# Kernel optimization log

Measured on AMD Instinct MI355X. Metric: run time of the kernel, lower is better.

Reference implementation:

```python
import jax, jax.numpy as jnp
import numpy as np

B, N, M = 4, 8192, 8192


def setup_inputs() -> dict:
    key = jax.random.key(0)
    k1, k2 = jax.random.split(key)
    xyz1 = jax.random.normal(k1, (B, N, 3), dtype=jnp.float32)
    xyz2 = jax.random.normal(k2, (B, M, 3), dtype=jnp.float32)
    return {"xyz1": xyz1, "xyz2": xyz2}


def reference(xyz1, xyz2):
    # Note: torch.cdist(p=2) returns sqrt(sq); min over sqrt == min over sq
    # (monotone), and the module squares afterward, so min of squared
    # distances is exactly equivalent (and avoids sqrt-at-0 grad issues).
    sq1 = jnp.sum(xyz1 * xyz1, axis=-1)  # (B, N)
    sq2 = jnp.sum(xyz2 * xyz2, axis=-1)  # (B, M)
    cross = jnp.einsum("bnd,bmd->bnm", xyz1, xyz2)  # (B, N, M)
    d2 = jnp.maximum(sq1[:, :, None] + sq2[:, None, :] - 2.0 * cross, 0.0)
    dist1 = jnp.min(d2, axis=2)  # (B, N) nearest in xyz2 for each xyz1 point
    dist2 = jnp.min(d2, axis=1)  # (B, M) nearest in xyz1 for each xyz2 point
    return jnp.mean(dist1) + jnp.mean(dist2)
```

## Files before the change

### kernel.cpp

```cpp
#include <hip/hip_runtime.h>
#include <math.h>

typedef short  bf16x8 __attribute__((ext_vector_type(8)));
typedef float  f32x16 __attribute__((ext_vector_type(16)));

constexpr int BATCH = 4, NPTS = 8192;
constexpr int CLOUD = BATCH * NPTS;

__device__ inline unsigned short bf16_rne(float x) {
    unsigned int u = __float_as_uint(x);
    return (unsigned short)((u + 0x7FFFu + ((u >> 16) & 1u)) >> 16);
}
__device__ inline float bf16_val(unsigned short h) {
    return __uint_as_float(((unsigned int)h) << 16);
}

__global__ __launch_bounds__(256) void cd_prep(
    const float* __restrict__ x1, const float* __restrict__ x2,
    uint4* __restrict__ APK, uint4* __restrict__ BPK,
    unsigned int* __restrict__ dist) {
    const int i = blockIdx.x * 256 + threadIdx.x;
    dist[i] = 0x7F800000u;
    const float* src = (i < CLOUD) ? x1 : x2;
    const int idx = i & (CLOUD - 1);
    const float x = src[idx*3+0], y = src[idx*3+1], z = src[idx*3+2];
    const float r = x*x + y*y + z*z;

    const unsigned short one = 0x3F80u;
    const unsigned short r0 = bf16_rne(r);
    const float rm1 = r - bf16_val(r0);
    const unsigned short r1 = bf16_rne(rm1);
    const unsigned short r2 = bf16_rne(rm1 - bf16_val(r1));

    const unsigned short hx = bf16_rne(x), hy = bf16_rne(y), hz = bf16_rne(z);
    const unsigned short lx = bf16_rne(x - bf16_val(hx));
    const unsigned short ly = bf16_rne(y - bf16_val(hy));
    const unsigned short lz = bf16_rne(z - bf16_val(hz));
    uint4 a0, a1;
    a0.x = (unsigned)hx | ((unsigned)lx << 16);
    a0.y = (unsigned)hx | ((unsigned)hy << 16);
    a0.z = (unsigned)ly | ((unsigned)hy << 16);
    a0.w = (unsigned)hz | ((unsigned)lz << 16);
    a1.x = (unsigned)hz | ((unsigned)one << 16);
    a1.y = (unsigned)one | ((unsigned)one << 16);
    a1.z = (unsigned)r0 | ((unsigned)r1 << 16);
    a1.w = (unsigned)r2;
    APK[2*i+0] = a0;  APK[2*i+1] = a1;

    const float tx = -2.f*x, ty = -2.f*y, tz = -2.f*z;
    const unsigned short ax = bf16_rne(tx), ay = bf16_rne(ty), az = bf16_rne(tz);
    const unsigned short bx = bf16_rne(tx - bf16_val(ax));
    const unsigned short by = bf16_rne(ty - bf16_val(ay));
    const unsigned short bz = bf16_rne(tz - bf16_val(az));
    uint4 b0, b1;
    b0.x = (unsigned)ax | ((unsigned)ax << 16);
    b0.y = (unsigned)bx | ((unsigned)ay << 16);
    b0.z = (unsigned)ay | ((unsigned)by << 16);
    b0.w = (unsigned)az | ((unsigned)az << 16);
    b1.x = (unsigned)bz | ((unsigned)r0 << 16);
    b1.y = (unsigned)r1 | ((unsigned)r2 << 16);
    b1.z = (unsigned)one | ((unsigned)one << 16);
    b1.w = (unsigned)one;
    BPK[2*i+0] = b0;  BPK[2*i+1] = b1;
}

__global__ __launch_bounds__(256) void cd_gemm(
    const uint4* __restrict__ APK, const uint4* __restrict__ BPK,
    unsigned int* __restrict__ dist) {

    __shared__ float lbuf[4][32][33];

    const int tid = threadIdx.x;
    const int wv  = tid >> 6;
    const int l   = tid & 63;
    const int lane31 = l & 31, half = l >> 5;

    const int wid = blockIdx.x * 4 + wv;
    const int dir = wid >> 12;
    const int b   = (wid >> 10) & 3;
    const int cc  = (wid >> 7) & 7;
    const int rg  = wid & 127;

    const int aBase = (dir ? CLOUD : 0) + b * NPTS + rg * 64;
    const int bBase = (dir ? 0 : CLOUD) + b * NPTS + cc * 1024;

    bf16x8 afr0, afr1;
    {
        uint4 v0 = APK[(size_t)(aBase + lane31) * 2 + half];
        uint4 v1 = APK[(size_t)(aBase + 32 + lane31) * 2 + half];
        __builtin_memcpy(&afr0, &v0, 16);
        __builtin_memcpy(&afr1, &v1, 16);
    }

    f32x16 zc;
#pragma unroll
    for (int i = 0; i < 16; ++i) zc[i] = 0.0f;

    float racc[2][16];
#pragma unroll
    for (int f = 0; f < 2; ++f)
#pragma unroll
        for (int r = 0; r < 16; ++r) racc[f][r] = INFINITY;

    uint4 u0, v0, u1, v1;
    const size_t bofs = (size_t)(bBase + lane31) * 2 + half;
#define CD_LD(U, V, PR) \
    U = BPK[bofs + (PR) * 128]; V = BPK[bofs + (PR) * 128 + 64];
#define CD_COMP(U, V)                                                        \
    {                                                                        \
        bf16x8 ba, bb;                                                       \
        __builtin_memcpy(&ba, &U, 16);                                       \
        __builtin_memcpy(&bb, &V, 16);                                       \
        f32x16 c0 = __builtin_amdgcn_mfma_f32_32x32x16_bf16(afr0, ba, zc, 0, 0, 0); \
        f32x16 c1 = __builtin_amdgcn_mfma_f32_32x32x16_bf16(afr0, bb, zc, 0, 0, 0); \
        f32x16 c2 = __builtin_amdgcn_mfma_f32_32x32x16_bf16(afr1, ba, zc, 0, 0, 0); \
        f32x16 c3 = __builtin_amdgcn_mfma_f32_32x32x16_bf16(afr1, bb, zc, 0, 0, 0); \
        _Pragma("unroll")                                                    \
        for (int r = 0; r < 16; ++r) {                                       \
            racc[0][r] = fminf(fminf(c0[r], c1[r]), racc[0][r]);             \
            racc[1][r] = fminf(fminf(c2[r], c3[r]), racc[1][r]);             \
        }                                                                    \
    }

    CD_LD(u0, v0, 0);
    for (int p = 0; p < 14; p += 2) {
        CD_LD(u1, v1, p + 1);
        CD_COMP(u0, v0);
        CD_LD(u0, v0, p + 2);
        CD_COMP(u1, v1);
    }
    CD_LD(u1, v1, 15);
    CD_COMP(u0, v0);
    CD_COMP(u1, v1);
#undef CD_LD
#undef CD_COMP

    const int distBase = dir * CLOUD + b * NPTS + rg * 64;
#pragma unroll
    for (int f = 0; f < 2; ++f) {
#pragma unroll
        for (int r = 0; r < 16; ++r) {
            const int rl = (r & 3) + 8 * (r >> 2) + 4 * half;
            lbuf[wv][rl][lane31] = racc[f][r];
        }
        const int row = l >> 1;
        float m = INFINITY;
#pragma unroll
        for (int i = 0; i < 16; ++i)
            m = fminf(m, lbuf[wv][row][(l & 1) * 16 + i]);
        m = fminf(m, __shfl_xor(m, 1, 64));
        if ((l & 1) == 0)
            atomicMin(&dist[distBase + f * 32 + row],
                      __float_as_uint(fmaxf(m, 0.0f)));
    }
}

__global__ __launch_bounds__(1024) void cd_reduce(
    const float* __restrict__ dm , float* __restrict__ out) {
    __shared__ float sw[16];
    const int t = threadIdx.x;
    const float4* v = reinterpret_cast<const float4*>(dm);
    float s = 0.0f;
#pragma unroll 4
    for (int i = t; i < 2 * CLOUD / 4; i += 1024) {
        float4 x = v[i];
        s += (x.x + x.y) + (x.z + x.w);
    }
#pragma unroll
    for (int off = 32; off > 0; off >>= 1) s += __shfl_down(s, off, 64);
    if ((t & 63) == 0) sw[t >> 6] = s;
    __syncthreads();
    if (t == 0) {
        float tot = 0.0f;
#pragma unroll
        for (int w = 0; w < 16; ++w) tot += sw[w];
        out[0] = tot / (float)CLOUD;
    }
}

extern "C" void kernel_launch(void* const* d_in, const int* in_sizes, int n_in,
                              void* d_out, int out_size, void* d_ws, size_t ws_size,
                              hipStream_t stream) {
    const float* xyz1 = (const float*)d_in[0];
    const float* xyz2 = (const float*)d_in[1];
    unsigned int* dist = (unsigned int*)d_ws;
    uint4* APK = (uint4*)((char*)d_ws + 2u * CLOUD * 4u);
    uint4* BPK = (uint4*)((char*)d_ws + 2u * CLOUD * 4u + 2u * CLOUD * 32u);
    float* out = (float*)d_out;

    cd_prep<<<2 * CLOUD / 256, 256, 0, stream>>>(xyz1, xyz2, APK, BPK, dist);
    cd_gemm<<<2048, 256, 0, stream>>>(APK, BPK, dist);
    cd_reduce<<<1, 1024, 0, stream>>>((const float*)dist, out);
}
```

Baseline: 40.43 us.

## Stage shared B tile in LDS and reorder packed layout for contiguous loads

The prep kernel now writes packed A/B fragments in a 32-point grouped layout, so each wave's fragment load is one contiguous 64-lane read. The gemm kernel loads the 1024-point B block once per workgroup into 32 KB of LDS, since all four waves share the same column chunk. The MFMA loop then reads B from LDS instead of each wave re-reading it from global memory. This cuts redundant global/L2 traffic but adds a barrier and LDS use per block, which may lower occupancy and drops the explicit register double-buffering.

After: 39.25 us. 1.03x faster.

```diff
diff --git a/kernel.cpp b/kernel.cpp
--- a/kernel.cpp
+++ b/kernel.cpp
@@ -45,7 +45,6 @@
     a1.y = (unsigned)one | ((unsigned)one << 16);
     a1.z = (unsigned)r0 | ((unsigned)r1 << 16);
     a1.w = (unsigned)r2;
-    APK[2*i+0] = a0;  APK[2*i+1] = a1;
 
     const float tx = -2.f*x, ty = -2.f*y, tz = -2.f*z;
     const unsigned short ax = bf16_rne(tx), ay = bf16_rne(ty), az = bf16_rne(tz);
@@ -61,13 +60,17 @@
     b1.y = (unsigned)r1 | ((unsigned)r2 << 16);
     b1.z = (unsigned)one | ((unsigned)one << 16);
     b1.w = (unsigned)one;
-    BPK[2*i+0] = b0;  BPK[2*i+1] = b1;
+
+    const int g = i >> 5, w = i & 31;
+    APK[g*64 + w]      = a0;  APK[g*64 + 32 + w] = a1;
+    BPK[g*64 + w]      = b0;  BPK[g*64 + 32 + w] = b1;
 }
 
 __global__ __launch_bounds__(256) void cd_gemm(
     const uint4* __restrict__ APK, const uint4* __restrict__ BPK,
     unsigned int* __restrict__ dist) {
 
+    __shared__ uint4 Blds[2048];
     __shared__ float lbuf[4][32][33];
 
     const int tid = threadIdx.x;
@@ -81,13 +84,20 @@
     const int cc  = (wid >> 7) & 7;
     const int rg  = wid & 127;
 
-    const int aBase = (dir ? CLOUD : 0) + b * NPTS + rg * 64;
-    const int bBase = (dir ? 0 : CLOUD) + b * NPTS + cc * 1024;
+    const int aPt = (dir ? CLOUD : 0) + b * NPTS + rg * 64;
+    const int bPt = (dir ? 0 : CLOUD) + b * NPTS + cc * 1024;
+
+    {
+        const uint4* src = BPK + (size_t)bPt * 2;
+#pragma unroll
+        for (int k = 0; k < 8; ++k)
+            Blds[tid + k * 256] = src[tid + k * 256];
+    }
 
     bf16x8 afr0, afr1;
     {
-        uint4 v0 = APK[(size_t)(aBase + lane31) * 2 + half];
-        uint4 v1 = APK[(size_t)(aBase + 32 + lane31) * 2 + half];
+        uint4 v0 = APK[(size_t)aPt * 2 + l];
+        uint4 v1 = APK[(size_t)aPt * 2 + 64 + l];
         __builtin_memcpy(&afr0, &v0, 16);
         __builtin_memcpy(&afr1, &v1, 16);
     }
@@ -102,38 +112,25 @@
 #pragma unroll
         for (int r = 0; r < 16; ++r) racc[f][r] = INFINITY;
 
-    uint4 u0, v0, u1, v1;
-    const size_t bofs = (size_t)(bBase + lane31) * 2 + half;
-#define CD_LD(U, V, PR) \
-    U = BPK[bofs + (PR) * 128]; V = BPK[bofs + (PR) * 128 + 64];
-#define CD_COMP(U, V)                                                        \
-    {                                                                        \
-        bf16x8 ba, bb;                                                       \
-        __builtin_memcpy(&ba, &U, 16);                                       \
-        __builtin_memcpy(&bb, &V, 16);                                       \
-        f32x16 c0 = __builtin_amdgcn_mfma_f32_32x32x16_bf16(afr0, ba, zc, 0, 0, 0); \
-        f32x16 c1 = __builtin_amdgcn_mfma_f32_32x32x16_bf16(afr0, bb, zc, 0, 0, 0); \
-        f32x16 c2 = __builtin_amdgcn_mfma_f32_32x32x16_bf16(afr1, ba, zc, 0, 0, 0); \
-        f32x16 c3 = __builtin_amdgcn_mfma_f32_32x32x16_bf16(afr1, bb, zc, 0, 0, 0); \
-        _Pragma("unroll")                                                    \
-        for (int r = 0; r < 16; ++r) {                                       \
-            racc[0][r] = fminf(fminf(c0[r], c1[r]), racc[0][r]);             \
-            racc[1][r] = fminf(fminf(c2[r], c3[r]), racc[1][r]);             \
-        }                                                                    \
+    __syncthreads();
+
+#pragma unroll 4
+    for (int p = 0; p < 16; ++p) {
+        bf16x8 ba, bb;
+        uint4 ua = Blds[(2*p + 0) * 64 + l];
+        uint4 ub = Blds[(2*p + 1) * 64 + l];
+        __builtin_memcpy(&ba, &ua, 16);
+        __builtin_memcpy(&bb, &ub, 16);
+        f32x16 c0 = __builtin_amdgcn_mfma_f32_32x32x16_bf16(afr0, ba, zc, 0, 0, 0);
+        f32x16 c1 = __builtin_amdgcn_mfma_f32_32x32x16_bf16(afr0, bb, zc, 0, 0, 0);
+        f32x16 c2 = __builtin_amdgcn_mfma_f32_32x32x16_bf16(afr1, ba, zc, 0, 0, 0);
+        f32x16 c3 = __builtin_amdgcn_mfma_f32_32x32x16_bf16(afr1, bb, zc, 0, 0, 0);
+#pragma unroll
+        for (int r = 0; r < 16; ++r) {
+            racc[0][r] = fminf(fminf(c0[r], c1[r]), racc[0][r]);
+            racc[1][r] = fminf(fminf(c2[r], c3[r]), racc[1][r]);
+        }
     }
-
-    CD_LD(u0, v0, 0);
-    for (int p = 0; p < 14; p += 2) {
-        CD_LD(u1, v1, p + 1);
-        CD_COMP(u0, v0);
-        CD_LD(u0, v0, p + 2);
-        CD_COMP(u1, v1);
-    }
-    CD_LD(u1, v1, 15);
-    CD_COMP(u0, v0);
-    CD_COMP(u1, v1);
-#undef CD_LD
-#undef CD_COMP
 
     const int distBase = dir * CLOUD + b * NPTS + rg * 64;
 #pragma unroll
```
